# Kernel tuning notes

Hardware: AMD Instinct MI355X
Metric: run time of the kernel (lower is better)

## Reference

```python
import jax, jax.numpy as jnp
import numpy as np

N_RAYS = 65536
N_SAMPLES = 128
LAST_DIST = 1e10  # effectively infinite final interval
EPS = 1e-10


def setup_inputs() -> dict:
    key = jax.random.key(0)
    k1, k2 = jax.random.split(key)
    raw = jax.random.normal(k1, (N_RAYS, N_SAMPLES, 4), dtype=jnp.float32)
    # monotonically increasing integration times per ray
    z_vals = jnp.sort(jax.random.uniform(k2, (N_RAYS, N_SAMPLES), dtype=jnp.float32) * 6.0 + 2.0, axis=-1)
    return {"raw": raw, "z_vals": z_vals}


def reference(raw, z_vals):
    # dists[i] = z[i+1] - z[i], last interval set to 1e10
    dists = jnp.concatenate(
        [z_vals[..., 1:] - z_vals[..., :-1],
         jnp.full_like(z_vals[..., :1], LAST_DIST)], axis=-1)  # [R, S]
    color = jax.nn.sigmoid(raw[..., :-1])                      # [R, S, 3]
    alpha = 1.0 - jnp.exp(-jax.nn.relu(raw[..., -1]) * dists)  # [R, S]
    # exclusive transmittance: T_i = prod_{j<i} (1 - alpha_j + eps), T_0 = 1
    trans = jnp.concatenate(
        [jnp.ones_like(alpha[..., :1]),
         jnp.cumprod(1.0 - alpha[..., :-1] + EPS, axis=-1)], axis=-1)  # [R, S]
    weights = alpha * trans                                    # [R, S]
    color_map = jnp.sum(weights[..., None] * color, axis=-2)   # [R, 3]
    return color_map
```

## Files before the change

kernel.cpp:

```cpp
#include <hip/hip_runtime.h>
#include <hip/hip_bf16.h>

#define N_SAMPLES 128
#define LAST_DIST 1e10f
#define EPS 1e-10f

__device__ __forceinline__ float sigmoidf(float x) {
    return 1.0f / (1.0f + expf(-x));
}

__global__ __launch_bounds__(256) void render_rays_kernel(
    const float4* __restrict__ raw,
    const float*  __restrict__ zv,
    float* __restrict__ out,
    int n_rays)
{
    const int wave_in_block = threadIdx.x >> 6;
    const int lane = threadIdx.x & 63;
    const int r = blockIdx.x * (blockDim.x >> 6) + wave_in_block;
    if (r >= n_rays) return;

    const size_t base = (size_t)r * N_SAMPLES;

    const float4 fa = raw[base + lane];
    const float4 fb = raw[base + 64 + lane];
    const float  za = zv[base + lane];
    const float  zb = zv[base + 64 + lane];

    const float za_next = __shfl_down(za, 1);
    const float zb_next = __shfl_down(zb, 1);
    const float z64     = __shfl(zb, 0);
    const float da = ((lane == 63) ? z64 : za_next) - za;
    const float db = (lane == 63) ? LAST_DIST : (zb_next - zb);

    const float ea = expf(-fmaxf(fa.w, 0.0f) * da);
    const float eb = expf(-fmaxf(fb.w, 0.0f) * db);
    const float ta = ea + EPS;
    const float tb = eb + EPS;

    float Pa = ta;
    #pragma unroll
    for (int off = 1; off < 64; off <<= 1) {
        const float v = __shfl_up(Pa, off);
        if (lane >= off) Pa *= v;
    }
    float Ta = __shfl_up(Pa, 1);
    if (lane == 0) Ta = 1.0f;
    const float total_a = __shfl(Pa, 63);

    float Pb = tb;
    #pragma unroll
    for (int off = 1; off < 64; off <<= 1) {
        const float v = __shfl_up(Pb, off);
        if (lane >= off) Pb *= v;
    }
    float Tb = __shfl_up(Pb, 1);
    if (lane == 0) Tb = 1.0f;
    Tb *= total_a;

    const float wa = (1.0f - ea) * Ta;
    const float wb = (1.0f - eb) * Tb;

    float accx = wa * sigmoidf(fa.x) + wb * sigmoidf(fb.x);
    float accy = wa * sigmoidf(fa.y) + wb * sigmoidf(fb.y);
    float accz = wa * sigmoidf(fa.z) + wb * sigmoidf(fb.z);

    #pragma unroll
    for (int off = 32; off > 0; off >>= 1) {
        accx += __shfl_xor(accx, off);
        accy += __shfl_xor(accy, off);
        accz += __shfl_xor(accz, off);
    }

    if (lane < 3) {
        out[(size_t)r * 3 + lane] = (lane == 0) ? accx : ((lane == 1) ? accy : accz);
    }
}

extern "C" void kernel_launch(void* const* d_in, const int* in_sizes, int n_in,
                              void* d_out, int out_size, void* d_ws, size_t ws_size,
                              hipStream_t stream) {
    const float4* raw = (const float4*)d_in[0];
    const float*  zv  = (const float*)d_in[1];
    float* out        = (float*)d_out;

    const int n_rays = in_sizes[0] / (N_SAMPLES * 4);

    const int waves_per_block = 4;
    const int block = waves_per_block * 64;
    const int grid = (n_rays + waves_per_block - 1) / waves_per_block;

    render_rays_kernel<<<grid, block, 0, stream>>>(raw, zv, out, n_rays);
}
```

Measured before the change: 206.1 us.

## Process four rays per wave with interleaved scans and fast sigmoid/exp intrinsics

Each wave now handles four rays, issuing all their global loads up front and interleaving the four independent prefix-product scans and reductions so shuffle latency overlaps across rays. Fast __expf and the hardware reciprocal replace expf and division in the sigmoid. A launch-bounds occupancy hint is added, and output writes are spread across lanes. The grid is four times smaller, which raises register pressure and may reduce the number of waves available to hide memory latency on a kernel that is largely bandwidth-bound.

```diff
diff --git a/kernel.cpp b/kernel.cpp
--- a/kernel.cpp
+++ b/kernel.cpp
@@ -4,76 +4,109 @@
 #define N_SAMPLES 128
 #define LAST_DIST 1e10f
 #define EPS 1e-10f
+#define RPW 4
 
-__device__ __forceinline__ float sigmoidf(float x) {
-    return 1.0f / (1.0f + expf(-x));
+__device__ __forceinline__ float fast_sigmoid(float x) {
+    return __builtin_amdgcn_rcpf(1.0f + __expf(-x));
 }
 
-__global__ __launch_bounds__(256) void render_rays_kernel(
+__global__ __launch_bounds__(256, 4) void render_rays_kernel(
     const float4* __restrict__ raw,
     const float*  __restrict__ zv,
     float* __restrict__ out,
     int n_rays)
 {
-    const int wave_in_block = threadIdx.x >> 6;
+    const int wave = threadIdx.x >> 6;
     const int lane = threadIdx.x & 63;
-    const int r = blockIdx.x * (blockDim.x >> 6) + wave_in_block;
-    if (r >= n_rays) return;
+    const int r0 = (blockIdx.x * (blockDim.x >> 6) + wave) * RPW;
+    if (r0 >= n_rays) return;
 
-    const size_t base = (size_t)r * N_SAMPLES;
+    float4 fa[RPW], fb[RPW];
+    float  za[RPW], zb[RPW];
+    #pragma unroll
+    for (int i = 0; i < RPW; ++i) {
+        const int ri = (r0 + i < n_rays) ? (r0 + i) : (n_rays - 1);
+        const size_t base = (size_t)ri * N_SAMPLES;
+        fa[i] = raw[base + lane];
+        fb[i] = raw[base + 64 + lane];
+        za[i] = zv[base + lane];
+        zb[i] = zv[base + 64 + lane];
+    }
 
-    const float4 fa = raw[base + lane];
-    const float4 fb = raw[base + 64 + lane];
-    const float  za = zv[base + lane];
-    const float  zb = zv[base + 64 + lane];
+    float ea[RPW], eb[RPW], Pa[RPW], Pb[RPW];
+    #pragma unroll
+    for (int i = 0; i < RPW; ++i) {
+        const float za_next = __shfl_down(za[i], 1);
+        const float zb_next = __shfl_down(zb[i], 1);
+        const float z64     = __shfl(zb[i], 0);
+        const float da = ((lane == 63) ? z64 : za_next) - za[i];
+        const float db = (lane == 63) ? LAST_DIST : (zb_next - zb[i]);
+        ea[i] = __expf(-fmaxf(fa[i].w, 0.0f) * da);
+        eb[i] = __expf(-fmaxf(fb[i].w, 0.0f) * db);
+        Pa[i] = ea[i] + EPS;
+        Pb[i] = eb[i] + EPS;
+    }
 
-    const float za_next = __shfl_down(za, 1);
-    const float zb_next = __shfl_down(zb, 1);
-    const float z64     = __shfl(zb, 0);
-    const float da = ((lane == 63) ? z64 : za_next) - za;
-    const float db = (lane == 63) ? LAST_DIST : (zb_next - zb);
-
-    const float ea = expf(-fmaxf(fa.w, 0.0f) * da);
-    const float eb = expf(-fmaxf(fb.w, 0.0f) * db);
-    const float ta = ea + EPS;
-    const float tb = eb + EPS;
-
-    float Pa = ta;
     #pragma unroll
     for (int off = 1; off < 64; off <<= 1) {
-        const float v = __shfl_up(Pa, off);
-        if (lane >= off) Pa *= v;
+        float v[RPW];
+        #pragma unroll
+        for (int i = 0; i < RPW; ++i) v[i] = __shfl_up(Pa[i], off);
+        #pragma unroll
+        for (int i = 0; i < RPW; ++i) if (lane >= off) Pa[i] *= v[i];
     }
-    float Ta = __shfl_up(Pa, 1);
-    if (lane == 0) Ta = 1.0f;
-    const float total_a = __shfl(Pa, 63);
+    float Ta[RPW], totA[RPW];
+    #pragma unroll
+    for (int i = 0; i < RPW; ++i) {
+        Ta[i] = __shfl_up(Pa[i], 1);
+        if (lane == 0) Ta[i] = 1.0f;
+        totA[i] = __shfl(Pa[i], 63);
+    }
 
-    float Pb = tb;
     #pragma unroll
     for (int off = 1; off < 64; off <<= 1) {
-        const float v = __shfl_up(Pb, off);
-        if (lane >= off) Pb *= v;
+        float v[RPW];
+        #pragma unroll
+        for (int i = 0; i < RPW; ++i) v[i] = __shfl_up(Pb[i], off);
+        #pragma unroll
+        for (int i = 0; i < RPW; ++i) if (lane >= off) Pb[i] *= v[i];
     }
-    float Tb = __shfl_up(Pb, 1);
-    if (lane == 0) Tb = 1.0f;
-    Tb *= total_a;
+    float Tb[RPW];
+    #pragma unroll
+    for (int i = 0; i < RPW; ++i) {
+        Tb[i] = __shfl_up(Pb[i], 1);
+        if (lane == 0) Tb[i] = 1.0f;
+        Tb[i] *= totA[i];
+    }
 
-    const float wa = (1.0f - ea) * Ta;
-    const float wb = (1.0f - eb) * Tb;
-
-    float accx = wa * sigmoidf(fa.x) + wb * sigmoidf(fb.x);
-    float accy = wa * sigmoidf(fa.y) + wb * sigmoidf(fb.y);
-    float accz = wa * sigmoidf(fa.z) + wb * sigmoidf(fb.z);
+    float acc[RPW][3];
+    #pragma unroll
+    for (int i = 0; i < RPW; ++i) {
+        const float wa = (1.0f - ea[i]) * Ta[i];
+        const float wb = (1.0f - eb[i]) * Tb[i];
+        acc[i][0] = wa * fast_sigmoid(fa[i].x) + wb * fast_sigmoid(fb[i].x);
+        acc[i][1] = wa * fast_sigmoid(fa[i].y) + wb * fast_sigmoid(fb[i].y);
+        acc[i][2] = wa * fast_sigmoid(fa[i].z) + wb * fast_sigmoid(fb[i].z);
+    }
 
     #pragma unroll
     for (int off = 32; off > 0; off >>= 1) {
-        accx += __shfl_xor(accx, off);
-        accy += __shfl_xor(accy, off);
-        accz += __shfl_xor(accz, off);
+        #pragma unroll
+        for (int i = 0; i < RPW; ++i) {
+            #pragma unroll
+            for (int c = 0; c < 3; ++c)
+                acc[i][c] += __shfl_xor(acc[i][c], off);
+        }
     }
 
-    if (lane < 3) {
-        out[(size_t)r * 3 + lane] = (lane == 0) ? accx : ((lane == 1) ? accy : accz);
+    #pragma unroll
+    for (int i = 0; i < RPW; ++i) {
+        if (lane == i * 16 && (r0 + i) < n_rays) {
+            const size_t o = (size_t)(r0 + i) * 3;
+            out[o + 0] = acc[i][0];
+            out[o + 1] = acc[i][1];
+            out[o + 2] = acc[i][2];
+        }
     }
 }
 
@@ -88,7 +121,8 @@
 
     const int waves_per_block = 4;
     const int block = waves_per_block * 64;
-    const int grid = (n_rays + waves_per_block - 1) / waves_per_block;
+    const int rays_per_block = waves_per_block * RPW;
+    const int grid = (n_rays + rays_per_block - 1) / rays_per_block;
 
     render_rays_kernel<<<grid, block, 0, stream>>>(raw, zv, out, n_rays);
 }
```

Result: slower. 211.4 us (+2.6%).

## Split each ray across four threads with serial segment compositing

Applied to the files above, without the earlier changes.

The work mapping changes from one 64-lane wave per ray, which ran two wave-wide shuffle scans, to four threads per ray. Each thread serially composites a contiguous 32-sample segment, and a small 4-lane shuffle scan then combines the segment transmittances. Precise expf and division are replaced by __expf and a hardware reciprocal, and z values are loaded as float4. The aim is to cut shuffle and scan overhead and keep many loads in flight per thread. The cost is strided, poorly coalesced per-instruction access across lanes and slightly lower numerical precision.

```diff
diff --git a/kernel.cpp b/kernel.cpp
--- a/kernel.cpp
+++ b/kernel.cpp
@@ -2,78 +2,73 @@
 #include <hip/hip_bf16.h>
 
 #define N_SAMPLES 128
+#define SEG 4
+#define SPT (N_SAMPLES / SEG)
 #define LAST_DIST 1e10f
 #define EPS 1e-10f
 
-__device__ __forceinline__ float sigmoidf(float x) {
-    return 1.0f / (1.0f + expf(-x));
+__device__ __forceinline__ float fast_sigmoid(float x) {
+    return __builtin_amdgcn_rcpf(1.0f + __expf(-x));
 }
 
-__global__ __launch_bounds__(256) void render_rays_kernel(
+__global__ __launch_bounds__(256, 2) void render_rays_kernel(
     const float4* __restrict__ raw,
-    const float*  __restrict__ zv,
+    const float4* __restrict__ z4,
     float* __restrict__ out,
     int n_rays)
 {
-    const int wave_in_block = threadIdx.x >> 6;
-    const int lane = threadIdx.x & 63;
-    const int r = blockIdx.x * (blockDim.x >> 6) + wave_in_block;
-    if (r >= n_rays) return;
+    const int tid = blockIdx.x * blockDim.x + threadIdx.x;
+    const int ray = tid >> 2;
+    const int q   = tid & 3;
+    if (ray >= n_rays) return;
 
-    const size_t base = (size_t)r * N_SAMPLES;
+    const size_t sbase = (size_t)ray * N_SAMPLES + (size_t)q * SPT;
+    const float4* rp = raw + sbase;
+    const float4* zp = z4 + (sbase >> 2);
 
-    const float4 fa = raw[base + lane];
-    const float4 fb = raw[base + 64 + lane];
-    const float  za = zv[base + lane];
-    const float  zb = zv[base + 64 + lane];
+    float zl[SPT];
+    #pragma unroll
+    for (int c = 0; c < SPT / 4; ++c) {
+        const float4 zv = zp[c];
+        zl[4 * c + 0] = zv.x;
+        zl[4 * c + 1] = zv.y;
+        zl[4 * c + 2] = zv.z;
+        zl[4 * c + 3] = zv.w;
+    }
+    const float z_bound = __shfl_down(zl[0], 1);
 
-    const float za_next = __shfl_down(za, 1);
-    const float zb_next = __shfl_down(zb, 1);
-    const float z64     = __shfl(zb, 0);
-    const float da = ((lane == 63) ? z64 : za_next) - za;
-    const float db = (lane == 63) ? LAST_DIST : (zb_next - zb);
-
-    const float ea = expf(-fmaxf(fa.w, 0.0f) * da);
-    const float eb = expf(-fmaxf(fb.w, 0.0f) * db);
-    const float ta = ea + EPS;
-    const float tb = eb + EPS;
-
-    float Pa = ta;
+    float T = 1.0f;
+    float cr = 0.0f, cg = 0.0f, cb = 0.0f;
     #pragma unroll
-    for (int off = 1; off < 64; off <<= 1) {
-        const float v = __shfl_up(Pa, off);
-        if (lane >= off) Pa *= v;
-    }
-    float Ta = __shfl_up(Pa, 1);
-    if (lane == 0) Ta = 1.0f;
-    const float total_a = __shfl(Pa, 63);
-
-    float Pb = tb;
-    #pragma unroll
-    for (int off = 1; off < 64; off <<= 1) {
-        const float v = __shfl_up(Pb, off);
-        if (lane >= off) Pb *= v;
-    }
-    float Tb = __shfl_up(Pb, 1);
-    if (lane == 0) Tb = 1.0f;
-    Tb *= total_a;
-
-    const float wa = (1.0f - ea) * Ta;
-    const float wb = (1.0f - eb) * Tb;
-
-    float accx = wa * sigmoidf(fa.x) + wb * sigmoidf(fb.x);
-    float accy = wa * sigmoidf(fa.y) + wb * sigmoidf(fb.y);
-    float accz = wa * sigmoidf(fa.z) + wb * sigmoidf(fb.z);
-
-    #pragma unroll
-    for (int off = 32; off > 0; off >>= 1) {
-        accx += __shfl_xor(accx, off);
-        accy += __shfl_xor(accy, off);
-        accz += __shfl_xor(accz, off);
+    for (int s = 0; s < SPT; ++s) {
+        const float4 f = rp[s];
+        float d;
+        if (s < SPT - 1)      d = zl[s + 1] - zl[s];
+        else if (q == SEG - 1) d = LAST_DIST;
+        else                   d = z_bound - zl[SPT - 1];
+        const float e = __expf(-fmaxf(f.w, 0.0f) * d);
+        const float w = (1.0f - e) * T;
+        cr = fmaf(w, fast_sigmoid(f.x), cr);
+        cg = fmaf(w, fast_sigmoid(f.y), cg);
+        cb = fmaf(w, fast_sigmoid(f.z), cb);
+        T *= (e + EPS);
     }
 
-    if (lane < 3) {
-        out[(size_t)r * 3 + lane] = (lane == 0) ? accx : ((lane == 1) ? accy : accz);
+    float Pinc = T;
+    float u = __shfl_up(Pinc, 1); if (q >= 1) Pinc *= u;
+    u       = __shfl_up(Pinc, 2); if (q >= 2) Pinc *= u;
+    float Tstart = __shfl_up(Pinc, 1);
+    if (q == 0) Tstart = 1.0f;
+
+    cr *= Tstart; cg *= Tstart; cb *= Tstart;
+    cr += __shfl_xor(cr, 1); cg += __shfl_xor(cg, 1); cb += __shfl_xor(cb, 1);
+    cr += __shfl_xor(cr, 2); cg += __shfl_xor(cg, 2); cb += __shfl_xor(cb, 2);
+
+    if (q == 0) {
+        const size_t o = (size_t)ray * 3;
+        out[o + 0] = cr;
+        out[o + 1] = cg;
+        out[o + 2] = cb;
     }
 }
 
@@ -81,14 +76,14 @@
                               void* d_out, int out_size, void* d_ws, size_t ws_size,
                               hipStream_t stream) {
     const float4* raw = (const float4*)d_in[0];
-    const float*  zv  = (const float*)d_in[1];
+    const float4* z4  = (const float4*)d_in[1];
     float* out        = (float*)d_out;
 
     const int n_rays = in_sizes[0] / (N_SAMPLES * 4);
 
-    const int waves_per_block = 4;
-    const int block = waves_per_block * 64;
-    const int grid = (n_rays + waves_per_block - 1) / waves_per_block;
+    const int block = 256;
+    const long long total_threads = (long long)n_rays * SEG;
+    const int grid = (int)((total_threads + block - 1) / block);
 
-    render_rays_kernel<<<grid, block, 0, stream>>>(raw, zv, out, n_rays);
+    render_rays_kernel<<<grid, block, 0, stream>>>(raw, z4, out, n_rays);
 }
```

New measurement: 222.8 us. 8.1% more time.
